# Kernel tuning notes

Hardware: AMD Instinct MI355X
Metric: run time of the kernel (lower is better)

The kernel has to match this reference:

```python
import jax, jax.numpy as jnp
import numpy as np

B, T, D, R = 16, 4096, 512, 256

# Buffers (match torch: linspace(0,T-1,R).long() truncates toward zero)
_LANDMARKS = np.linspace(0.0, T - 1, R).astype(np.int64)
_POS = np.arange(T)[:, None]                                   # [T,1]
_MASK = (_LANDMARKS[None, :] < _POS)                           # [T,R] bool: landmark j < position i
_TDIST = np.clip((_POS.astype(np.float32) - _LANDMARKS[None, :].astype(np.float32)) / T, 0.0, None).astype(np.float32)  # [T,R]


def setup_inputs() -> dict:
    key = jax.random.key(0)
    k1, k2, k3 = jax.random.split(key, 3)
    return {
        "z": jax.random.normal(k1, (B, T, D), dtype=jnp.float32),
        "gegenbauer_weights": jax.random.normal(k2, (3,), dtype=jnp.float32),
        "temporal_alpha": jax.random.normal(k3, (1,), dtype=jnp.float32),
    }


def reference(z, gegenbauer_weights, temporal_alpha):
    dtype = z.dtype
    mask = jnp.asarray(_MASK)                       # [T,R]
    tdist = jnp.asarray(_TDIST, dtype=dtype)        # [T,R]
    lm = jnp.asarray(_LANDMARKS)                    # [R]

    # F.normalize(z, dim=-1) with eps=1e-12
    norm = jnp.linalg.norm(z, axis=-1, keepdims=True)
    Q = z / jnp.maximum(norm, 1e-12)                # [B,T,D]
    K = Q[:, lm, :]                                 # [B,R,D]
    C = jnp.einsum('btd,brd->btr', Q, K)            # [B,T,R] cosine similarity

    # Gegenbauer mixture
    alpha = jax.nn.softmax(gegenbauer_weights)
    C2 = C * C
    P1 = (1.0 + C) * 0.5
    P2 = (3.0 * C2 - 1.0) * 0.5
    P3 = (5.0 * C2 * C - 3.0 * C) * 0.5
    Phi = alpha[0] * P1 + alpha[1] * P2 + alpha[2] * P3

    # Causal mask
    Phi = Phi * mask.astype(dtype)[None, :, :]

    # Temporal decay
    a_td = jax.nn.softplus(temporal_alpha[0])
    Phi = Phi * jnp.exp(-a_td * tdist)[None, :, :]

    # Row-sum normalization
    row_sum = jnp.maximum(Phi.sum(axis=-1, keepdims=True), 1e-6)
    Phi = Phi / row_sum

    # Append constant-ones feature -> [B,T,R+1]
    ones = jnp.ones((Phi.shape[0], Phi.shape[1], 1), dtype=dtype)
    return jnp.concatenate([Phi, ones], axis=-1)
```

## Files before the change

kernel.cpp:

```cpp
#include <hip/hip_runtime.h>
#include <hip/hip_bf16.h>
#include <math.h>

#define B_DIM 16
#define T_DIM 4096
#define D_DIM 512
#define R_DIM 256

#define TM 64
#define BK 32
#define LDAP 40
#define LDBP 40

typedef __bf16 bf16x8 __attribute__((ext_vector_type(8)));
typedef float floatx4 __attribute__((ext_vector_type(4)));

__device__ __forceinline__ int landmark_of(int r) {
    if (r >= 255) return 4095;
    const double step = 4095.0 / 255.0;
    return (int)((double)r * step);
}

__device__ __forceinline__ void split_bf16(float x, __bf16& h, __bf16& l) {
    h = (__bf16)x;
    l = (__bf16)(x - (float)h);
}

__global__ void nystrom_prep_kernel(const float* __restrict__ z,
                                    __bf16* __restrict__ Khi, __bf16* __restrict__ Klo) {
    int blk = blockIdx.x;
    int b = blk >> 8;
    int r = blk & 255;
    int lane = threadIdx.x;
    int lm = landmark_of(r);
    const float* src = z + ((size_t)b * T_DIM + lm) * D_DIM + lane * 8;
    float4 v0 = ((const float4*)src)[0];
    float4 v1 = ((const float4*)src)[1];
    float ss = v0.x*v0.x + v0.y*v0.y + v0.z*v0.z + v0.w*v0.w
             + v1.x*v1.x + v1.y*v1.y + v1.z*v1.z + v1.w*v1.w;
    #pragma unroll
    for (int off = 1; off < 64; off <<= 1) ss += __shfl_xor(ss, off, 64);
    float inv = 1.0f / fmaxf(sqrtf(ss), 1e-12f);
    float q[8] = {v0.x*inv, v0.y*inv, v0.z*inv, v0.w*inv,
                  v1.x*inv, v1.y*inv, v1.z*inv, v1.w*inv};
    bf16x8 oh, ol;
    #pragma unroll
    for (int j = 0; j < 8; j++) { __bf16 h, l; split_bf16(q[j], h, l); oh[j] = h; ol[j] = l; }
    size_t dst = ((size_t)b * R_DIM + r) * D_DIM + lane * 8;
    *(bf16x8*)(Khi + dst) = oh;
    *(bf16x8*)(Klo + dst) = ol;
}

__global__ __launch_bounds__(256, 2)
void nystrom_main_kernel(const float* __restrict__ z,
                         const __bf16* __restrict__ Khi, const __bf16* __restrict__ Klo,
                         const float* __restrict__ gw, const float* __restrict__ ta,
                         float* __restrict__ out) {
    __shared__ __attribute__((aligned(16))) __bf16 Ash[TM * LDAP];
    __shared__ __attribute__((aligned(16))) __bf16 Asl[TM * LDAP];
    __shared__ __attribute__((aligned(16))) __bf16 Bsh[R_DIM * LDBP];
    __shared__ __attribute__((aligned(16))) __bf16 Bsl[R_DIM * LDBP];
    __shared__ float red[256];
    __shared__ float rnorm[TM];
    __shared__ float rspart[4][TM];
    __shared__ float rinv[TM];
    __shared__ int   lmtab[R_DIM];
    __shared__ float elmtab[R_DIM];

    const int tid  = threadIdx.x;
    const int b    = blockIdx.y;
    const int t0   = blockIdx.x * TM;
    const int lane = tid & 63;
    const int wv   = tid >> 6;
    const int quad = lane >> 4;
    const int ln   = lane & 15;

    float g0 = gw[0], g1 = gw[1], g2 = gw[2];
    float gm = fmaxf(g0, fmaxf(g1, g2));
    float e0 = expf(g0 - gm), e1 = expf(g1 - gm), e2 = expf(g2 - gm);
    float esum = e0 + e1 + e2;
    float al0 = e0 / esum, al1 = e1 / esum, al2 = e2 / esum;
    float ax = ta[0];
    float a_td = (ax > 20.f) ? ax : log1pf(expf(ax));

    if (tid < R_DIM) {
        int lm = landmark_of(tid);
        lmtab[tid] = lm;
        elmtab[tid] = expf(a_td * (float)lm * (1.0f / 4096.0f));
    }

    const int srowA = tid >> 2;
    const int scolA = (tid & 3) * 8;
    const float*  zrow = z + ((size_t)b * T_DIM + (t0 + srowA)) * D_DIM + scolA;
    const size_t  kboff = (size_t)b * R_DIM * D_DIM;
    const __bf16* Kbh = Khi + kboff;
    const __bf16* Kbl = Klo + kboff;

    floatx4 acc[4][4];
    #pragma unroll
    for (int i = 0; i < 4; i++)
        #pragma unroll
        for (int j = 0; j < 4; j++) acc[i][j] = (floatx4){0.f, 0.f, 0.f, 0.f};
    float ssq = 0.0f;

    for (int kt = 0; kt < D_DIM; kt += BK) {
        float4 a0 = *(const float4*)(zrow + kt + 0);
        float4 a1 = *(const float4*)(zrow + kt + 4);
        float av[8] = {a0.x, a0.y, a0.z, a0.w, a1.x, a1.y, a1.z, a1.w};
        #pragma unroll
        for (int j = 0; j < 8; j++) ssq += av[j] * av[j];
        bf16x8 ph, pl;
        #pragma unroll
        for (int j = 0; j < 8; j++) { __bf16 h, l; split_bf16(av[j], h, l); ph[j] = h; pl[j] = l; }
        *(bf16x8*)&Ash[srowA * LDAP + scolA] = ph;
        *(bf16x8*)&Asl[srowA * LDAP + scolA] = pl;
        {
            const __bf16* bph = Kbh + (size_t)tid * D_DIM + kt;
            const __bf16* bpl = Kbl + (size_t)tid * D_DIM + kt;
            uint4 h0 = ((const uint4*)bph)[0], h1 = ((const uint4*)bph)[1];
            uint4 h2 = ((const uint4*)bph)[2], h3 = ((const uint4*)bph)[3];
            uint4 l0 = ((const uint4*)bpl)[0], l1 = ((const uint4*)bpl)[1];
            uint4 l2 = ((const uint4*)bpl)[2], l3 = ((const uint4*)bpl)[3];
            uint4* dh = (uint4*)&Bsh[tid * LDBP];
            uint4* dl = (uint4*)&Bsl[tid * LDBP];
            dh[0] = h0; dh[1] = h1;
            ((uint4*)((char*)&Bsh[0] + tid * 80))[0] = h0;
            ((uint4*)((char*)&Bsh[0] + tid * 80))[1] = h1;
            ((uint4*)((char*)&Bsh[0] + tid * 80))[2] = h2;
            ((uint4*)((char*)&Bsh[0] + tid * 80))[3] = h3;
            ((uint4*)((char*)&Bsl[0] + tid * 80))[0] = l0;
            ((uint4*)((char*)&Bsl[0] + tid * 80))[1] = l1;
            ((uint4*)((char*)&Bsl[0] + tid * 80))[2] = l2;
            ((uint4*)((char*)&Bsl[0] + tid * 80))[3] = l3;
        }
        __syncthreads();
        {
            int koff = quad * 8;
            bf16x8 afh[4], afl[4], bfh[4], bfl[4];
            #pragma unroll
            for (int mi = 0; mi < 4; mi++) {
                afh[mi] = *(const bf16x8*)&Ash[(mi * 16 + ln) * LDAP + koff];
                afl[mi] = *(const bf16x8*)&Asl[(mi * 16 + ln) * LDAP + koff];
            }
            #pragma unroll
            for (int ni = 0; ni < 4; ni++) {
                bfh[ni] = *(const bf16x8*)&Bsh[(wv * 64 + ni * 16 + ln) * LDBP + koff];
                bfl[ni] = *(const bf16x8*)&Bsl[(wv * 64 + ni * 16 + ln) * LDBP + koff];
            }
            #pragma unroll
            for (int mi = 0; mi < 4; mi++)
                #pragma unroll
                for (int ni = 0; ni < 4; ni++) {
                    acc[mi][ni] = __builtin_amdgcn_mfma_f32_16x16x32_bf16(
                        afh[mi], bfh[ni], acc[mi][ni], 0, 0, 0);
                    acc[mi][ni] = __builtin_amdgcn_mfma_f32_16x16x32_bf16(
                        afh[mi], bfl[ni], acc[mi][ni], 0, 0, 0);
                    acc[mi][ni] = __builtin_amdgcn_mfma_f32_16x16x32_bf16(
                        afl[mi], bfh[ni], acc[mi][ni], 0, 0, 0);
                }
        }
        __syncthreads();
    }

    red[tid] = ssq;
    __syncthreads();
    if (tid < TM) {
        float s = red[tid*4] + red[tid*4+1] + red[tid*4+2] + red[tid*4+3];
        rnorm[tid] = 1.0f / fmaxf(sqrtf(s), 1e-12f);
    }
    __syncthreads();

    int   lm_r[4];
    float elm_r[4];
    #pragma unroll
    for (int ni = 0; ni < 4; ni++) {
        int r = wv * 64 + ni * 16 + ln;
        lm_r[ni]  = lmtab[r];
        elm_r[ni] = elmtab[r];
    }

    #pragma unroll
    for (int mi = 0; mi < 4; mi++) {
        #pragma unroll
        for (int reg = 0; reg < 4; reg++) {
            int row = mi * 16 + quad * 4 + reg;
            int t = t0 + row;
            float rn = rnorm[row];
            float e_t = expf(-a_td * (float)t * (1.0f / 4096.0f));
            float s = 0.f;
            #pragma unroll
            for (int ni = 0; ni < 4; ni++) {
                float phi = 0.f;
                if (lm_r[ni] < t) {
                    float c  = acc[mi][ni][reg] * rn;
                    float c2 = c * c;
                    float P1 = 0.5f * (1.f + c);
                    float P2 = 0.5f * (3.f * c2 - 1.f);
                    float P3 = 0.5f * (5.f * c2 * c - 3.f * c);
                    float p  = al0 * P1 + al1 * P2 + al2 * P3;
                    phi = p * e_t * elm_r[ni];
                }
                acc[mi][ni][reg] = phi;
                s += phi;
            }
            #pragma unroll
            for (int off = 1; off < 16; off <<= 1) s += __shfl_xor(s, off, 64);
            if (ln == 0) rspart[wv][row] = s;
        }
    }
    __syncthreads();
    if (tid < TM) {
        float rs = rspart[0][tid] + rspart[1][tid] + rspart[2][tid] + rspart[3][tid];
        rinv[tid] = 1.0f / fmaxf(rs, 1e-6f);
    }
    __syncthreads();

    float* ob = out + ((size_t)b * T_DIM + t0) * 257;
    #pragma unroll
    for (int mi = 0; mi < 4; mi++) {
        #pragma unroll
        for (int reg = 0; reg < 4; reg++) {
            int row = mi * 16 + quad * 4 + reg;
            float inv = rinv[row];
            #pragma unroll
            for (int ni = 0; ni < 4; ni++) {
                int r = wv * 64 + ni * 16 + ln;
                ob[(size_t)row * 257 + r] = acc[mi][ni][reg] * inv;
            }
        }
    }
    if (tid < TM) ob[(size_t)tid * 257 + 256] = 1.0f;
}

extern "C" void kernel_launch(void* const* d_in, const int* in_sizes, int n_in,
                              void* d_out, int out_size, void* d_ws, size_t ws_size,
                              hipStream_t stream) {
    const float* z  = (const float*)d_in[0];
    const float* gw = (const float*)d_in[1];
    const float* ta = (const float*)d_in[2];
    float* out = (float*)d_out;
    __bf16* Khi = (__bf16*)d_ws;
    __bf16* Klo = (__bf16*)((char*)d_ws + (size_t)B_DIM * R_DIM * D_DIM * 2);

    nystrom_prep_kernel<<<dim3(B_DIM * R_DIM), 64, 0, stream>>>(z, Khi, Klo);
    nystrom_main_kernel<<<dim3(T_DIM / TM, B_DIM), 256, 0, stream>>>(z, Khi, Klo, gw, ta, out);
}
```

Measured before the change: 309.4 us.

## Double the row tile, chunk the landmark layout, and prefetch next K-slice into registers

The row tile grows from 64 to 128 so each block reuses the staged landmark hi/lo tiles across twice as many rows, halving global landmark traffic per output. The prep kernel now writes the landmark matrix in a per-32-column chunked layout so each K-step load is contiguous, and the next slice of z and landmarks is prefetched into registers before the MFMA loop. Shared memory is unified into one reused buffer. This doubles accumulator registers (128 floats) and may lower occupancy or cause spills under launch_bounds(256,2); the grid also halves to 512 blocks.

```diff
diff --git a/kernel.cpp b/kernel.cpp
--- a/kernel.cpp
+++ b/kernel.cpp
@@ -7,10 +7,10 @@
 #define D_DIM 512
 #define R_DIM 256
 
-#define TM 64
+#define TM 128
 #define BK 32
-#define LDAP 40
-#define LDBP 40
+#define LDP 40
+#define NKCH (D_DIM/BK)
 
 typedef __bf16 bf16x8 __attribute__((ext_vector_type(8)));
 typedef float floatx4 __attribute__((ext_vector_type(4)));
@@ -46,7 +46,7 @@
     bf16x8 oh, ol;
     #pragma unroll
     for (int j = 0; j < 8; j++) { __bf16 h, l; split_bf16(q[j], h, l); oh[j] = h; ol[j] = l; }
-    size_t dst = ((size_t)b * R_DIM + r) * D_DIM + lane * 8;
+    size_t dst = (((size_t)b * NKCH + (lane >> 2)) * R_DIM + r) * BK + (size_t)(lane & 3) * 8;
     *(bf16x8*)(Khi + dst) = oh;
     *(bf16x8*)(Klo + dst) = ol;
 }
@@ -56,16 +56,18 @@
                          const __bf16* __restrict__ Khi, const __bf16* __restrict__ Klo,
                          const float* __restrict__ gw, const float* __restrict__ ta,
                          float* __restrict__ out) {
-    __shared__ __attribute__((aligned(16))) __bf16 Ash[TM * LDAP];
-    __shared__ __attribute__((aligned(16))) __bf16 Asl[TM * LDAP];
-    __shared__ __attribute__((aligned(16))) __bf16 Bsh[R_DIM * LDBP];
-    __shared__ __attribute__((aligned(16))) __bf16 Bsl[R_DIM * LDBP];
-    __shared__ float red[256];
-    __shared__ float rnorm[TM];
-    __shared__ float rspart[4][TM];
-    __shared__ float rinv[TM];
+    __shared__ __attribute__((aligned(16))) char smem[61440];
     __shared__ int   lmtab[R_DIM];
     __shared__ float elmtab[R_DIM];
+
+    __bf16* Ash = (__bf16*)(smem);
+    __bf16* Asl = (__bf16*)(smem + 10240);
+    __bf16* Bsh = (__bf16*)(smem + 20480);
+    __bf16* Bsl = (__bf16*)(smem + 40960);
+    float* red    = (float*)(smem);
+    float* rnormp = (float*)(smem + 1024);
+    float* rinvp  = (float*)(smem + 1536);
+    float* rspart = (float*)(smem + 2048);
 
     const int tid  = threadIdx.x;
     const int b    = blockIdx.y;
@@ -83,81 +85,89 @@
     float ax = ta[0];
     float a_td = (ax > 20.f) ? ax : log1pf(expf(ax));
 
-    if (tid < R_DIM) {
+    {
         int lm = landmark_of(tid);
         lmtab[tid] = lm;
         elmtab[tid] = expf(a_td * (float)lm * (1.0f / 4096.0f));
     }
 
-    const int srowA = tid >> 2;
-    const int scolA = (tid & 3) * 8;
-    const float*  zrow = z + ((size_t)b * T_DIM + (t0 + srowA)) * D_DIM + scolA;
-    const size_t  kboff = (size_t)b * R_DIM * D_DIM;
-    const __bf16* Kbh = Khi + kboff;
-    const __bf16* Kbl = Klo + kboff;
-
-    floatx4 acc[4][4];
-    #pragma unroll
-    for (int i = 0; i < 4; i++)
+    const int srowA = tid >> 1;
+    const int scolA = (tid & 1) * 16;
+    const float* zrow = z + ((size_t)b * T_DIM + (t0 + srowA)) * D_DIM + scolA;
+    const size_t bbase = (size_t)b * NKCH * R_DIM * BK;
+
+    floatx4 acc[8][4];
+    #pragma unroll
+    for (int i = 0; i < 8; i++)
         #pragma unroll
         for (int j = 0; j < 4; j++) acc[i][j] = (floatx4){0.f, 0.f, 0.f, 0.f};
     float ssq = 0.0f;
 
+    float4 a0, a1, a2, a3;
+    uint4 h0, h1, h2, h3, l0, l1, l2, l3;
+    {
+        const float4* ap = (const float4*)(zrow);
+        a0 = ap[0]; a1 = ap[1]; a2 = ap[2]; a3 = ap[3];
+        const uint4* ph = (const uint4*)(Khi + bbase + (size_t)tid * BK);
+        const uint4* pl = (const uint4*)(Klo + bbase + (size_t)tid * BK);
+        h0 = ph[0]; h1 = ph[1]; h2 = ph[2]; h3 = ph[3];
+        l0 = pl[0]; l1 = pl[1]; l2 = pl[2]; l3 = pl[3];
+    }
+
+    #pragma unroll 1
     for (int kt = 0; kt < D_DIM; kt += BK) {
-        float4 a0 = *(const float4*)(zrow + kt + 0);
-        float4 a1 = *(const float4*)(zrow + kt + 4);
-        float av[8] = {a0.x, a0.y, a0.z, a0.w, a1.x, a1.y, a1.z, a1.w};
-        #pragma unroll
-        for (int j = 0; j < 8; j++) ssq += av[j] * av[j];
-        bf16x8 ph, pl;
-        #pragma unroll
-        for (int j = 0; j < 8; j++) { __bf16 h, l; split_bf16(av[j], h, l); ph[j] = h; pl[j] = l; }
-        *(bf16x8*)&Ash[srowA * LDAP + scolA] = ph;
-        *(bf16x8*)&Asl[srowA * LDAP + scolA] = pl;
+        float av[16] = {a0.x,a0.y,a0.z,a0.w, a1.x,a1.y,a1.z,a1.w,
+                        a2.x,a2.y,a2.z,a2.w, a3.x,a3.y,a3.z,a3.w};
+        #pragma unroll
+        for (int j = 0; j < 16; j++) ssq += av[j] * av[j];
+        bf16x8 ph0, pl0, ph1, pl1;
+        #pragma unroll
+        for (int j = 0; j < 8; j++) { __bf16 h, l; split_bf16(av[j],   h, l); ph0[j]=h; pl0[j]=l; }
+        #pragma unroll
+        for (int j = 0; j < 8; j++) { __bf16 h, l; split_bf16(av[8+j], h, l); ph1[j]=h; pl1[j]=l; }
+        *(bf16x8*)&Ash[srowA * LDP + scolA]     = ph0;
+        *(bf16x8*)&Ash[srowA * LDP + scolA + 8] = ph1;
+        *(bf16x8*)&Asl[srowA * LDP + scolA]     = pl0;
+        *(bf16x8*)&Asl[srowA * LDP + scolA + 8] = pl1;
         {
-            const __bf16* bph = Kbh + (size_t)tid * D_DIM + kt;
-            const __bf16* bpl = Kbl + (size_t)tid * D_DIM + kt;
-            uint4 h0 = ((const uint4*)bph)[0], h1 = ((const uint4*)bph)[1];
-            uint4 h2 = ((const uint4*)bph)[2], h3 = ((const uint4*)bph)[3];
-            uint4 l0 = ((const uint4*)bpl)[0], l1 = ((const uint4*)bpl)[1];
-            uint4 l2 = ((const uint4*)bpl)[2], l3 = ((const uint4*)bpl)[3];
-            uint4* dh = (uint4*)&Bsh[tid * LDBP];
-            uint4* dl = (uint4*)&Bsl[tid * LDBP];
-            dh[0] = h0; dh[1] = h1;
-            ((uint4*)((char*)&Bsh[0] + tid * 80))[0] = h0;
-            ((uint4*)((char*)&Bsh[0] + tid * 80))[1] = h1;
-            ((uint4*)((char*)&Bsh[0] + tid * 80))[2] = h2;
-            ((uint4*)((char*)&Bsh[0] + tid * 80))[3] = h3;
-            ((uint4*)((char*)&Bsl[0] + tid * 80))[0] = l0;
-            ((uint4*)((char*)&Bsl[0] + tid * 80))[1] = l1;
-            ((uint4*)((char*)&Bsl[0] + tid * 80))[2] = l2;
-            ((uint4*)((char*)&Bsl[0] + tid * 80))[3] = l3;
+            uint4* dh = (uint4*)((char*)Bsh + tid * (LDP * 2));
+            uint4* dl = (uint4*)((char*)Bsl + tid * (LDP * 2));
+            dh[0] = h0; dh[1] = h1; dh[2] = h2; dh[3] = h3;
+            dl[0] = l0; dl[1] = l1; dl[2] = l2; dl[3] = l3;
         }
         __syncthreads();
+        if (kt + BK < D_DIM) {
+            const float4* ap = (const float4*)(zrow + kt + BK);
+            a0 = ap[0]; a1 = ap[1]; a2 = ap[2]; a3 = ap[3];
+            size_t coff = bbase + (size_t)((kt >> 5) + 1) * R_DIM * BK + (size_t)tid * BK;
+            const uint4* ph = (const uint4*)(Khi + coff);
+            const uint4* pl = (const uint4*)(Klo + coff);
+            h0 = ph[0]; h1 = ph[1]; h2 = ph[2]; h3 = ph[3];
+            l0 = pl[0]; l1 = pl[1]; l2 = pl[2]; l3 = pl[3];
+        }
         {
-            int koff = quad * 8;
-            bf16x8 afh[4], afl[4], bfh[4], bfl[4];
-            #pragma unroll
-            for (int mi = 0; mi < 4; mi++) {
-                afh[mi] = *(const bf16x8*)&Ash[(mi * 16 + ln) * LDAP + koff];
-                afl[mi] = *(const bf16x8*)&Asl[(mi * 16 + ln) * LDAP + koff];
-            }
+            const int koff = quad * 8;
+            bf16x8 bfh[4], bfl[4];
             #pragma unroll
             for (int ni = 0; ni < 4; ni++) {
-                bfh[ni] = *(const bf16x8*)&Bsh[(wv * 64 + ni * 16 + ln) * LDBP + koff];
-                bfl[ni] = *(const bf16x8*)&Bsl[(wv * 64 + ni * 16 + ln) * LDBP + koff];
-            }
-            #pragma unroll
-            for (int mi = 0; mi < 4; mi++)
+                int rrow = wv * 64 + ni * 16 + ln;
+                bfh[ni] = *(const bf16x8*)&Bsh[rrow * LDP + koff];
+                bfl[ni] = *(const bf16x8*)&Bsl[rrow * LDP + koff];
+            }
+            #pragma unroll
+            for (int mi = 0; mi < 8; mi++) {
+                bf16x8 afh = *(const bf16x8*)&Ash[(mi * 16 + ln) * LDP + koff];
+                bf16x8 afl = *(const bf16x8*)&Asl[(mi * 16 + ln) * LDP + koff];
                 #pragma unroll
                 for (int ni = 0; ni < 4; ni++) {
                     acc[mi][ni] = __builtin_amdgcn_mfma_f32_16x16x32_bf16(
-                        afh[mi], bfh[ni], acc[mi][ni], 0, 0, 0);
+                        afh, bfh[ni], acc[mi][ni], 0, 0, 0);
                     acc[mi][ni] = __builtin_amdgcn_mfma_f32_16x16x32_bf16(
-                        afh[mi], bfl[ni], acc[mi][ni], 0, 0, 0);
+                        afh, bfl[ni], acc[mi][ni], 0, 0, 0);
                     acc[mi][ni] = __builtin_amdgcn_mfma_f32_16x16x32_bf16(
-                        afl[mi], bfh[ni], acc[mi][ni], 0, 0, 0);
+                        afl, bfh[ni], acc[mi][ni], 0, 0, 0);
                 }
+            }
         }
         __syncthreads();
     }
@@ -165,8 +175,8 @@
     red[tid] = ssq;
     __syncthreads();
     if (tid < TM) {
-        float s = red[tid*4] + red[tid*4+1] + red[tid*4+2] + red[tid*4+3];
-        rnorm[tid] = 1.0f / fmaxf(sqrtf(s), 1e-12f);
+        float s = red[tid * 2] + red[tid * 2 + 1];
+        rnormp[tid] = 1.0f / fmaxf(sqrtf(s), 1e-12f);
     }
     __syncthreads();
 
@@ -180,12 +190,12 @@
     }
 
     #pragma unroll
-    for (int mi = 0; mi < 4; mi++) {
+    for (int mi = 0; mi < 8; mi++) {
         #pragma unroll
         for (int reg = 0; reg < 4; reg++) {
             int row = mi * 16 + quad * 4 + reg;
             int t = t0 + row;
-            float rn = rnorm[row];
+            float rn = rnormp[row];
             float e_t = expf(-a_td * (float)t * (1.0f / 4096.0f));
             float s = 0.f;
             #pragma unroll
@@ -205,23 +215,24 @@
             }
             #pragma unroll
             for (int off = 1; off < 16; off <<= 1) s += __shfl_xor(s, off, 64);
-            if (ln == 0) rspart[wv][row] = s;
+            if (ln == 0) rspart[wv * TM + row] = s;
         }
     }
     __syncthreads();
     if (tid < TM) {
-        float rs = rspart[0][tid] + rspart[1][tid] + rspart[2][tid] + rspart[3][tid];
-        rinv[tid] = 1.0f / fmaxf(rs, 1e-6f);
+        float rs = rspart[0 * TM + tid] + rspart[1 * TM + tid]
+                 + rspart[2 * TM + tid] + rspart[3 * TM + tid];
+        rinvp[tid] = 1.0f / fmaxf(rs, 1e-6f);
     }
     __syncthreads();
 
     float* ob = out + ((size_t)b * T_DIM + t0) * 257;
     #pragma unroll
-    for (int mi = 0; mi < 4; mi++) {
+    for (int mi = 0; mi < 8; mi++) {
         #pragma unroll
         for (int reg = 0; reg < 4; reg++) {
             int row = mi * 16 + quad * 4 + reg;
-            float inv = rinv[row];
+            float inv = rinvp[row];
             #pragma unroll
             for (int ni = 0; ni < 4; ni++) {
                 int r = wv * 64 + ni * 16 + ln;
```

Measured after the change: 252.2 us. 1.23x faster.

## Pre-swizzle landmark tiles and stream them into LDS via async global_load_lds

Applied to the files above, without the earlier changes.

The prep kernel now writes the normalized landmark hi/lo bf16 splits into per-K-chunk blobs with an XOR-style rotated layout that matches the LDS layout. The main kernel copies each chunk directly into LDS using global_load_lds, prefetches the next z slice into registers, and uses a rotated, unpadded A layout to avoid bank conflicts. Shared memory drops to about 40KB, which allows occupancy of 3 blocks per CU, and the small lookup tables and reductions move to registers and shuffles. It still uses a single LDS buffer with two barriers per K step, so the async copies are not double-buffered.

```diff
diff --git a/kernel.cpp b/kernel.cpp
--- a/kernel.cpp
+++ b/kernel.cpp
@@ -9,8 +9,8 @@
 
 #define TM 64
 #define BK 32
-#define LDAP 40
-#define LDBP 40
+#define NKCH 16
+#define CHUNK 32768
 
 typedef __bf16 bf16x8 __attribute__((ext_vector_type(8)));
 typedef float floatx4 __attribute__((ext_vector_type(4)));
@@ -26,8 +26,13 @@
     l = (__bf16)(x - (float)h);
 }
 
-__global__ void nystrom_prep_kernel(const float* __restrict__ z,
-                                    __bf16* __restrict__ Khi, __bf16* __restrict__ Klo) {
+__device__ __forceinline__ void async_copy16(const void* g, void* l) {
+    __builtin_amdgcn_global_load_lds(
+        (const __attribute__((address_space(1))) unsigned int*)g,
+        (__attribute__((address_space(3))) unsigned int*)l, 16, 0, 0);
+}
+
+__global__ void nystrom_prep_kernel(const float* __restrict__ z, char* __restrict__ blob) {
     int blk = blockIdx.x;
     int b = blk >> 8;
     int r = blk & 255;
@@ -41,38 +46,33 @@
     #pragma unroll
     for (int off = 1; off < 64; off <<= 1) ss += __shfl_xor(ss, off, 64);
     float inv = 1.0f / fmaxf(sqrtf(ss), 1e-12f);
-    float q[8] = {v0.x*inv, v0.y*inv, v0.z*inv, v0.w*inv,
-                  v1.x*inv, v1.y*inv, v1.z*inv, v1.w*inv};
+    float qv[8] = {v0.x*inv, v0.y*inv, v0.z*inv, v0.w*inv,
+                   v1.x*inv, v1.y*inv, v1.z*inv, v1.w*inv};
     bf16x8 oh, ol;
     #pragma unroll
-    for (int j = 0; j < 8; j++) { __bf16 h, l; split_bf16(q[j], h, l); oh[j] = h; ol[j] = l; }
-    size_t dst = ((size_t)b * R_DIM + r) * D_DIM + lane * 8;
-    *(bf16x8*)(Khi + dst) = oh;
-    *(bf16x8*)(Klo + dst) = ol;
-}
-
-__global__ __launch_bounds__(256, 2)
-void nystrom_main_kernel(const float* __restrict__ z,
-                         const __bf16* __restrict__ Khi, const __bf16* __restrict__ Klo,
+    for (int j = 0; j < 8; j++) { __bf16 h, l; split_bf16(qv[j], h, l); oh[j] = h; ol[j] = l; }
+    int kc = lane >> 2, g = lane & 3;
+    char* dst = blob + ((size_t)(b * NKCH + kc)) * CHUNK + r * 64 + 16 * ((g + r) & 3);
+    *(bf16x8*)dst = oh;
+    *(bf16x8*)(dst + 16384) = ol;
+}
+
+__global__ __launch_bounds__(256, 3)
+void nystrom_main_kernel(const float* __restrict__ z, const char* __restrict__ blob,
                          const float* __restrict__ gw, const float* __restrict__ ta,
                          float* __restrict__ out) {
-    __shared__ __attribute__((aligned(16))) __bf16 Ash[TM * LDAP];
-    __shared__ __attribute__((aligned(16))) __bf16 Asl[TM * LDAP];
-    __shared__ __attribute__((aligned(16))) __bf16 Bsh[R_DIM * LDBP];
-    __shared__ __attribute__((aligned(16))) __bf16 Bsl[R_DIM * LDBP];
-    __shared__ float red[256];
-    __shared__ float rnorm[TM];
-    __shared__ float rspart[4][TM];
-    __shared__ float rinv[TM];
-    __shared__ int   lmtab[R_DIM];
-    __shared__ float elmtab[R_DIM];
+    __shared__ __attribute__((aligned(16))) char smem[40960];
+    __bf16* Bs = (__bf16*)smem;
+    char*   Asb = smem + 32768;
+    float* rnorm_s = (float*)(smem + 32768);
+    float* rspart  = (float*)(smem + 32768 + 256);
 
     const int tid  = threadIdx.x;
     const int b    = blockIdx.y;
     const int t0   = blockIdx.x * TM;
     const int lane = tid & 63;
     const int wv   = tid >> 6;
-    const int quad = lane >> 4;
+    const int q    = lane >> 4;
     const int ln   = lane & 15;
 
     float g0 = gw[0], g1 = gw[1], g2 = gw[2];
@@ -83,18 +83,13 @@
     float ax = ta[0];
     float a_td = (ax > 20.f) ? ax : log1pf(expf(ax));
 
-    if (tid < R_DIM) {
-        int lm = landmark_of(tid);
-        lmtab[tid] = lm;
-        elmtab[tid] = expf(a_td * (float)lm * (1.0f / 4096.0f));
-    }
-
-    const int srowA = tid >> 2;
-    const int scolA = (tid & 3) * 8;
-    const float*  zrow = z + ((size_t)b * T_DIM + (t0 + srowA)) * D_DIM + scolA;
-    const size_t  kboff = (size_t)b * R_DIM * D_DIM;
-    const __bf16* Kbh = Khi + kboff;
-    const __bf16* Kbl = Klo + kboff;
+    const int arow = tid >> 2, ag = tid & 3;
+    const float* zsrc = z + ((size_t)b * T_DIM + t0 + arow) * D_DIM + ag * 8;
+    char* awh = Asb + arow * 64 + 16 * ((ag + arow) & 3);
+    char* awl = awh + 4096;
+
+    const char* bsrc0 = blob + (size_t)(b * NKCH) * CHUNK + wv * 8192 + lane * 16;
+    char* bdst0 = smem + wv * 8192;
 
     floatx4 acc[4][4];
     #pragma unroll
@@ -103,71 +98,64 @@
         for (int j = 0; j < 4; j++) acc[i][j] = (floatx4){0.f, 0.f, 0.f, 0.f};
     float ssq = 0.0f;
 
-    for (int kt = 0; kt < D_DIM; kt += BK) {
-        float4 a0 = *(const float4*)(zrow + kt + 0);
-        float4 a1 = *(const float4*)(zrow + kt + 4);
-        float av[8] = {a0.x, a0.y, a0.z, a0.w, a1.x, a1.y, a1.z, a1.w};
-        #pragma unroll
-        for (int j = 0; j < 8; j++) ssq += av[j] * av[j];
-        bf16x8 ph, pl;
-        #pragma unroll
-        for (int j = 0; j < 8; j++) { __bf16 h, l; split_bf16(av[j], h, l); ph[j] = h; pl[j] = l; }
-        *(bf16x8*)&Ash[srowA * LDAP + scolA] = ph;
-        *(bf16x8*)&Asl[srowA * LDAP + scolA] = pl;
+    float4 pa0 = *(const float4*)(zsrc);
+    float4 pa1 = *(const float4*)(zsrc + 4);
+
+    #pragma unroll 1
+    for (int kt = 0; kt < NKCH; kt++) {
         {
-            const __bf16* bph = Kbh + (size_t)tid * D_DIM + kt;
-            const __bf16* bpl = Kbl + (size_t)tid * D_DIM + kt;
-            uint4 h0 = ((const uint4*)bph)[0], h1 = ((const uint4*)bph)[1];
-            uint4 h2 = ((const uint4*)bph)[2], h3 = ((const uint4*)bph)[3];
-            uint4 l0 = ((const uint4*)bpl)[0], l1 = ((const uint4*)bpl)[1];
-            uint4 l2 = ((const uint4*)bpl)[2], l3 = ((const uint4*)bpl)[3];
-            uint4* dh = (uint4*)&Bsh[tid * LDBP];
-            uint4* dl = (uint4*)&Bsl[tid * LDBP];
-            dh[0] = h0; dh[1] = h1;
-            ((uint4*)((char*)&Bsh[0] + tid * 80))[0] = h0;
-            ((uint4*)((char*)&Bsh[0] + tid * 80))[1] = h1;
-            ((uint4*)((char*)&Bsh[0] + tid * 80))[2] = h2;
-            ((uint4*)((char*)&Bsh[0] + tid * 80))[3] = h3;
-            ((uint4*)((char*)&Bsl[0] + tid * 80))[0] = l0;
-            ((uint4*)((char*)&Bsl[0] + tid * 80))[1] = l1;
-            ((uint4*)((char*)&Bsl[0] + tid * 80))[2] = l2;
-            ((uint4*)((char*)&Bsl[0] + tid * 80))[3] = l3;
+            float av[8] = {pa0.x, pa0.y, pa0.z, pa0.w, pa1.x, pa1.y, pa1.z, pa1.w};
+            bf16x8 h8, l8;
+            #pragma unroll
+            for (int j = 0; j < 8; j++) {
+                ssq += av[j] * av[j];
+                __bf16 h, l; split_bf16(av[j], h, l); h8[j] = h; l8[j] = l;
+            }
+            *(bf16x8*)awh = h8;
+            *(bf16x8*)awl = l8;
+        }
+        {
+            const char* bs = bsrc0 + (size_t)kt * CHUNK;
+            #pragma unroll
+            for (int i = 0; i < 8; i++)
+                async_copy16(bs + i * 1024, bdst0 + i * 1024);
         }
         __syncthreads();
+
+        if (kt + 1 < NKCH) {
+            const float* zp = zsrc + (kt + 1) * BK;
+            pa0 = *(const float4*)(zp);
+            pa1 = *(const float4*)(zp + 4);
+        }
+
         {
-            int koff = quad * 8;
-            bf16x8 afh[4], afl[4], bfh[4], bfl[4];
+            const int rot = 16 * ((q + ln) & 3);
+            bf16x8 bh[4], bl[4];
+            #pragma unroll
+            for (int ni = 0; ni < 4; ni++) {
+                const char* p = (const char*)Bs + (wv * 64 + ni * 16 + ln) * 64 + rot;
+                bh[ni] = *(const bf16x8*)p;
+                bl[ni] = *(const bf16x8*)(p + 16384);
+            }
             #pragma unroll
             for (int mi = 0; mi < 4; mi++) {
-                afh[mi] = *(const bf16x8*)&Ash[(mi * 16 + ln) * LDAP + koff];
-                afl[mi] = *(const bf16x8*)&Asl[(mi * 16 + ln) * LDAP + koff];
-            }
-            #pragma unroll
-            for (int ni = 0; ni < 4; ni++) {
-                bfh[ni] = *(const bf16x8*)&Bsh[(wv * 64 + ni * 16 + ln) * LDBP + koff];
-                bfl[ni] = *(const bf16x8*)&Bsl[(wv * 64 + ni * 16 + ln) * LDBP + koff];
-            }
-            #pragma unroll
-            for (int mi = 0; mi < 4; mi++)
+                const char* pa = Asb + (mi * 16 + ln) * 64 + rot;
+                bf16x8 ah = *(const bf16x8*)pa;
+                bf16x8 al = *(const bf16x8*)(pa + 4096);
                 #pragma unroll
                 for (int ni = 0; ni < 4; ni++) {
-                    acc[mi][ni] = __builtin_amdgcn_mfma_f32_16x16x32_bf16(
-                        afh[mi], bfh[ni], acc[mi][ni], 0, 0, 0);
-                    acc[mi][ni] = __builtin_amdgcn_mfma_f32_16x16x32_bf16(
-                        afh[mi], bfl[ni], acc[mi][ni], 0, 0, 0);
-                    acc[mi][ni] = __builtin_amdgcn_mfma_f32_16x16x32_bf16(
-                        afl[mi], bfh[ni], acc[mi][ni], 0, 0, 0);
+                    acc[mi][ni] = __builtin_amdgcn_mfma_f32_16x16x32_bf16(ah, bh[ni], acc[mi][ni], 0, 0, 0);
+                    acc[mi][ni] = __builtin_amdgcn_mfma_f32_16x16x32_bf16(ah, bl[ni], acc[mi][ni], 0, 0, 0);
+                    acc[mi][ni] = __builtin_amdgcn_mfma_f32_16x16x32_bf16(al, bh[ni], acc[mi][ni], 0, 0, 0);
                 }
+            }
         }
         __syncthreads();
     }
 
-    red[tid] = ssq;
-    __syncthreads();
-    if (tid < TM) {
-        float s = red[tid*4] + red[tid*4+1] + red[tid*4+2] + red[tid*4+3];
-        rnorm[tid] = 1.0f / fmaxf(sqrtf(s), 1e-12f);
-    }
+    ssq += __shfl_xor(ssq, 1, 64);
+    ssq += __shfl_xor(ssq, 2, 64);
+    if (ag == 0) rnorm_s[arow] = 1.0f / fmaxf(sqrtf(ssq), 1e-12f);
     __syncthreads();
 
     int   lm_r[4];
@@ -175,18 +163,18 @@
     #pragma unroll
     for (int ni = 0; ni < 4; ni++) {
         int r = wv * 64 + ni * 16 + ln;
-        lm_r[ni]  = lmtab[r];
-        elm_r[ni] = elmtab[r];
+        lm_r[ni]  = landmark_of(r);
+        elm_r[ni] = expf(a_td * (float)lm_r[ni] * (1.0f / 4096.0f));
     }
 
     #pragma unroll
     for (int mi = 0; mi < 4; mi++) {
         #pragma unroll
         for (int reg = 0; reg < 4; reg++) {
-            int row = mi * 16 + quad * 4 + reg;
-            int t = t0 + row;
-            float rn = rnorm[row];
-            float e_t = expf(-a_td * (float)t * (1.0f / 4096.0f));
+            const int row = mi * 16 + q * 4 + reg;
+            const int t = t0 + row;
+            const float rn = rnorm_s[row];
+            const float e_t = expf(-a_td * (float)t * (1.0f / 4096.0f));
             float s = 0.f;
             #pragma unroll
             for (int ni = 0; ni < 4; ni++) {
@@ -203,15 +191,12 @@
                 acc[mi][ni][reg] = phi;
                 s += phi;
             }
-            #pragma unroll
-            for (int off = 1; off < 16; off <<= 1) s += __shfl_xor(s, off, 64);
-            if (ln == 0) rspart[wv][row] = s;
-        }
-    }
-    __syncthreads();
-    if (tid < TM) {
-        float rs = rspart[0][tid] + rspart[1][tid] + rspart[2][tid] + rspart[3][tid];
-        rinv[tid] = 1.0f / fmaxf(rs, 1e-6f);
+            s += __shfl_xor(s, 1, 64);
+            s += __shfl_xor(s, 2, 64);
+            s += __shfl_xor(s, 4, 64);
+            s += __shfl_xor(s, 8, 64);
+            if (ln == 0) rspart[wv * 64 + row] = s;
+        }
     }
     __syncthreads();
 
@@ -220,12 +205,12 @@
     for (int mi = 0; mi < 4; mi++) {
         #pragma unroll
         for (int reg = 0; reg < 4; reg++) {
-            int row = mi * 16 + quad * 4 + reg;
-            float inv = rinv[row];
+            const int row = mi * 16 + q * 4 + reg;
+            float rs = rspart[row] + rspart[64 + row] + rspart[128 + row] + rspart[192 + row];
+            float inv = 1.0f / fmaxf(rs, 1e-6f);
             #pragma unroll
             for (int ni = 0; ni < 4; ni++) {
-                int r = wv * 64 + ni * 16 + ln;
-                ob[(size_t)row * 257 + r] = acc[mi][ni][reg] * inv;
+                ob[(size_t)row * 257 + wv * 64 + ni * 16 + ln] = acc[mi][ni][reg] * inv;
             }
         }
     }
@@ -239,9 +224,8 @@
     const float* gw = (const float*)d_in[1];
     const float* ta = (const float*)d_in[2];
     float* out = (float*)d_out;
-    __bf16* Khi = (__bf16*)d_ws;
-    __bf16* Klo = (__bf16*)((char*)d_ws + (size_t)B_DIM * R_DIM * D_DIM * 2);
-
-    nystrom_prep_kernel<<<dim3(B_DIM * R_DIM), 64, 0, stream>>>(z, Khi, Klo);
-    nystrom_main_kernel<<<dim3(T_DIM / TM, B_DIM), 256, 0, stream>>>(z, Khi, Klo, gw, ta, out);
-}
+    char* blob = (char*)d_ws;
+
+    nystrom_prep_kernel<<<dim3(B_DIM * R_DIM), 64, 0, stream>>>(z, blob);
+    nystrom_main_kernel<<<dim3(T_DIM / TM, B_DIM), 256, 0, stream>>>(z, blob, gw, ta, out);
+}
```

Result: faster. 270.2 us (-12.7%).
